# Performance work log

Hardware: AMD Instinct MI355X
Metric: run time of the kernel (lower is better)

The kernel has to match this reference:

```python
import jax, jax.numpy as jnp
import numpy as np

# LIF constants from the source module
ALPHA = float(np.exp(-0.001 / 0.005))  # synaptic decay
BETA = float(np.exp(-0.001 / 0.01))    # membrane decay
TH = 1.0
SCALE = 100.0

@jax.custom_vjp
def spike(x):
    return (x > 0).astype(x.dtype)

def _spike_fwd(x):
    return spike(x), x

def _spike_bwd(x, g):
    return (g / (1.0 + SCALE * jnp.abs(x)) ** 2,)

spike.defvjp(_spike_fwd, _spike_bwd)

T, NI, NH, NO = 1000, 700, 4096, 20

def setup_inputs() -> dict:
    key = jax.random.key(0)
    k1, k2, k3, k4 = jax.random.split(key, 4)
    input_spikes = (jax.random.uniform(k1, (T, NI)) < 0.1).astype(jnp.float32)
    # nn.Linear default init: U(-1/sqrt(fan_in), 1/sqrt(fan_in)), weight shape [out, in]
    s_in = 1.0 / np.sqrt(NI)
    s_fb = 1.0 / np.sqrt(NH)
    W_in = jax.random.uniform(k2, (NH, NI), minval=-s_in, maxval=s_in, dtype=jnp.float32)
    W_fb = jax.random.uniform(k3, (NH, NH), minval=-s_fb, maxval=s_fb, dtype=jnp.float32)
    W_ro = jax.random.uniform(k4, (NO, NH), minval=-s_fb, maxval=s_fb, dtype=jnp.float32)
    return {"input_spikes": input_spikes, "W_in": W_in, "W_fb": W_fb, "W_ro": W_ro}

def reference(input_spikes, W_in, W_fb, W_ro):
    nh = W_in.shape[0]
    no = W_ro.shape[0]

    def step(carry, inp):
        mem1, syn1, out1, mem2, syn2 = carry
        # input + feedback synaptic current (feedback uses previous step spikes)
        cur = W_in @ inp + W_fb @ out1
        # hidden LIF: reset where previous out spiked (detached), spike, decay
        rst = jax.lax.stop_gradient(out1)
        mem1 = mem1 * (1.0 - rst)
        out1_new = spike(mem1 - TH)
        mem1_new = mem1 * BETA + syn1
        syn1_new = syn1 * ALPHA + cur
        # readout LIF: no reset; recorded mem is pre-integration of current input
        ro_cur = W_ro @ out1_new
        mem2_new = mem2 * BETA + syn2
        syn2_new = syn2 * ALPHA + ro_cur
        return (mem1_new, syn1_new, out1_new, mem2_new, syn2_new), mem2_new

    carry0 = (jnp.zeros(nh, input_spikes.dtype), jnp.zeros(nh, input_spikes.dtype),
              jnp.zeros(nh, input_spikes.dtype), jnp.zeros(no, input_spikes.dtype),
              jnp.zeros(no, input_spikes.dtype))
    _, ro_mem_rec = jax.lax.scan(step, carry0, input_spikes)  # [T, num_output]
    return ro_mem_rec.T  # torch.stack(..., dim=1) -> [num_output, T]
```

## Files before the change

kernel.cpp:

```cpp
#include <hip/hip_runtime.h>

#define T_STEPS 1000
#define NI 700
#define NIQ 11
#define NH 4096
#define NO 20

#define ALPHA 0.8187307530779818f
#define BETA  0.9048374180359595f

#define NBH 64
#define BLOCK 1024
#define NWAVE 16
#define SPW 4
#define SLOTW 16
#define NCH 6
#define CAP (NCH * 8)
#define WLCAP 328
#define ZROW NI
#define NROWS (NI + 1 + NH)

typedef unsigned long long u64;
typedef unsigned int u32;
typedef int v4i __attribute__((ext_vector_type(4)));

__device__ __forceinline__ void pub16(u32* p, v4i v)
{
    asm volatile("global_store_dwordx4 %0, %1, off sc0 sc1"
                 :: "v"((u64)(uintptr_t)p), "v"(v) : "memory");
}
__device__ __forceinline__ v4i poll16(const u32* p)
{
    v4i r;
    asm volatile("global_load_dwordx4 %0, %1, off sc0 sc1\n\ts_waitcnt vmcnt(0)"
                 : "=v"(r) : "v"((u64)(uintptr_t)p) : "memory");
    return r;
}

__global__ void __launch_bounds__(256)
tpose_kernel(const float* __restrict__ in, float* __restrict__ out, int R, int C)
{
    __shared__ float tile[32][33];
    const int c  = blockIdx.x * 32 + threadIdx.x;
    const int r0 = blockIdx.y * 32;
    for (int dy = threadIdx.y; dy < 32; dy += 8) {
        const int r = r0 + dy;
        if (r < R && c < C) tile[dy][threadIdx.x] = in[(size_t)r * C + c];
    }
    __syncthreads();
    const int r2 = r0 + threadIdx.x;
    for (int dy = threadIdx.y; dy < 32; dy += 8) {
        const int c2 = blockIdx.x * 32 + dy;
        if (c2 < C && r2 < R) out[(size_t)c2 * R + r2] = tile[threadIdx.x][dy];
    }
}

__global__ void __launch_bounds__(256)
inpmask_kernel(const float* __restrict__ in, u64* __restrict__ msk)
{
    const int t    = blockIdx.x * 4 + (threadIdx.x >> 6);
    const int lane = threadIdx.x & 63;
    if (t >= T_STEPS) return;
    const float* __restrict__ row = in + (size_t)t * NI;
    for (int q = 0; q < NIQ; ++q) {
        const int j = q * 64 + lane;
        const u64 m = __ballot(j < NI && row[j] > 0.5f);
        if (lane == 0) msk[t * 16 + q] = m;
    }
}

__global__ void __launch_bounds__(BLOCK)
snn_kernel(const u64*  __restrict__ inpMask,
           const float* __restrict__ W_ro,
           const float* __restrict__ Wall,
           float* __restrict__ out,
           u32*   __restrict__ mb)
{
    const int tid  = threadIdx.x;
    const int lane = tid & 63;
    const int w    = tid >> 6;
    const int b    = blockIdx.x;

    if (b == NBH) {
        __shared__ int actR[NH];
        __shared__ int actRn;
        float mem2 = 0.f, syn2 = 0.f;

        for (int t = 0; t < T_STEPS; ++t) {
            if (w == 0) {
                const u32* tg = &mb[((size_t)t * NBH + lane) * SLOTW];
                v4i r;
                do { r = poll16(tg); } while ((u32)r.z != (u32)(t + 1));
                const u64 m = ((u64)(u32)r.y << 32) | (u32)r.x;
                const int cnt = __popcll(m);
                int v = cnt;
                #pragma unroll
                for (int d = 1; d < 64; d <<= 1) {
                    const int u = __shfl_up(v, d, 64);
                    if (lane >= d) v += u;
                }
                int o = v - cnt;
                if (lane == 63) actRn = v;
                u64 mm = m;
                const int base = lane * 64;
                while (mm) {
                    const int bit = __builtin_ctzll(mm);
                    mm &= mm - 1;
                    actR[o++] = base + bit;
                }
            }
            __syncthreads();

            const int nR = actRn;
            if (tid < NO * 32) {
                const int o = tid >> 5, k = tid & 31;
                const float* __restrict__ Wr = W_ro + o * NH;
                float r0 = 0.f, r1 = 0.f, r2 = 0.f, r3 = 0.f;
                int n = k;
                for (; n + 96 < nR; n += 128) {
                    r0 += Wr[actR[n]];      r1 += Wr[actR[n + 32]];
                    r2 += Wr[actR[n + 64]]; r3 += Wr[actR[n + 96]];
                }
                for (; n < nR; n += 32) r0 += Wr[actR[n]];
                float rc = (r0 + r1) + (r2 + r3);
                #pragma unroll
                for (int d = 16; d; d >>= 1) rc += __shfl_xor(rc, d, 32);
                if (k == 0) {
                    const float m2n = mem2 * BETA + syn2;
                    out[o * T_STEPS + t] = m2n;
                    syn2 = syn2 * ALPHA + rc;
                    mem2 = m2n;
                }
            }
            __syncthreads();
        }
        return;
    }

    __shared__ float pcur[2][BLOCK];
    __shared__ int   wl[2][NWAVE][WLCAP];

    const int i   = b * 64 + lane;
    const int bb0 = w * SPW;
    const int qw  = (w >= NWAVE - NIQ) ? (w - (NWAVE - NIQ)) : -1;
    const float* __restrict__ WallC = Wall + i;

    float M = 0.f, S = 0.f, o_prev = 0.f, o_cur = 0.f;
    float pf[CAP];
    int prevCnt = 0;

    if (w == 0 && lane == 0) {
        v4i pkt; pkt.x = 0; pkt.y = 0; pkt.z = 1; pkt.w = 0;
        pub16(&mb[(size_t)b * SLOTW], pkt);
    }

    for (int k = 0; k < T_STEPS; ++k) {
        const int pb = (k + 1) & 1;

        {
            float s0 = 0.f, s1 = 0.f, s2 = 0.f, s3 = 0.f;
            #pragma unroll
            for (int c = 0; c < NCH; ++c) {
                if (prevCnt > c * 8) {
                    s0 += pf[c*8+0]; s1 += pf[c*8+1];
                    s2 += pf[c*8+2]; s3 += pf[c*8+3];
                    s0 += pf[c*8+4]; s1 += pf[c*8+5];
                    s2 += pf[c*8+6]; s3 += pf[c*8+7];
                }
            }
            for (int n = CAP; n < prevCnt; ++n)
                s0 += WallC[(size_t)wl[pb & 1][w][n] * NH];
            pcur[pb][tid] = (s0 + s1) + (s2 + s3);
        }

        int cnt = 0;
        int* mylist = wl[k & 1][w];
        if (qw >= 0) {
            const u64 m = inpMask[(size_t)k * 16 + qw];
            if ((m >> lane) & 1)
                mylist[__popcll(m & (((u64)1 << lane) - 1))] = qw * 64 + lane;
            cnt = __popcll(m);
        }

        if (k > 0) {
            u64 mk = 0;
            if (lane < SPW) {
                const u32* tg = &mb[((size_t)(k - 1) * NBH + bb0 + lane) * SLOTW];
                v4i r;
                do { r = poll16(tg); } while ((u32)r.z != (u32)k);
                mk = ((u64)(u32)r.y << 32) | (u32)r.x;
            }
            #pragma unroll
            for (int s = 0; s < SPW; ++s) {
                const u64 m = __shfl(mk, s, 64);
                if ((m >> lane) & 1)
                    mylist[cnt + __popcll(m & (((u64)1 << lane) - 1))]
                        = NI + 1 + (bb0 + s) * 64 + lane;
                cnt += __popcll(m);
            }
        }
        const int padded = (cnt + 7) & ~7;
        if (lane < padded - cnt) mylist[cnt + lane] = ZROW;
        prevCnt = padded;

        #pragma unroll
        for (int c = 0; c < NCH; ++c) {
            if (padded > c * 8) {
                #pragma unroll
                for (int q = 0; q < 8; ++q)
                    pf[c*8+q] = WallC[(size_t)mylist[c*8+q] * NH];
            }
        }

        asm volatile("s_waitcnt lgkmcnt(0)\n\ts_barrier" ::: "memory");

        if (w == 0) {
            float cur = 0.f;
            #pragma unroll
            for (int ww = 0; ww < NWAVE; ++ww) cur += pcur[pb][lane + 64 * ww];
            S = S * ALPHA + cur;
            const float Mr = M * (1.f - o_prev);
            M = Mr * BETA + S;
            const float on = (M * (1.f - o_cur) > 1.f) ? 1.f : 0.f;
            o_prev = o_cur; o_cur = on;
            const u64 sm = __ballot(on > 0.f);
            if (lane == 0) {
                v4i pkt;
                pkt.x = (int)(u32)sm;
                pkt.y = (int)(u32)(sm >> 32);
                pkt.z = (int)(u32)(k + 2);
                pkt.w = 0;
                pub16(&mb[((size_t)(k + 1) * NBH + b) * SLOTW], pkt);
            }
        }
    }
}

extern "C" void kernel_launch(void* const* d_in, const int* in_sizes, int n_in,
                              void* d_out, int out_size, void* d_ws, size_t ws_size,
                              hipStream_t stream)
{
    const float* inp  = (const float*)d_in[0];
    const float* W_in = (const float*)d_in[1];
    const float* W_fb = (const float*)d_in[2];
    const float* W_ro = (const float*)d_in[3];
    float* out = (float*)d_out;

    char* ws = (char*)d_ws;
    size_t off = 0;
    auto alloc = [&](size_t bytes) -> void* {
        void* p = ws + off;
        off = (off + bytes + 255) & ~(size_t)255;
        return p;
    };
    float* Wall    = (float*)alloc(sizeof(float) * (size_t)NROWS * NH);
    u64*   inpMask = (u64*)alloc(sizeof(u64) * (size_t)T_STEPS * 16);
    u32*   mb      = (u32*)alloc(sizeof(u32) * (size_t)(T_STEPS + 1) * NBH * SLOTW);

    (void)hipMemsetAsync(mb, 0, sizeof(u32) * (size_t)(T_STEPS + 1) * NBH * SLOTW, stream);
    (void)hipMemsetAsync(Wall + (size_t)ZROW * NH, 0, sizeof(float) * NH, stream);

    dim3 tb(32, 8);
    tpose_kernel<<<dim3((NH + 31) / 32, (NH + 31) / 32), tb, 0, stream>>>(
        W_in, Wall, NH, NI);
    tpose_kernel<<<dim3((NH + 31) / 32, (NH + 31) / 32), tb, 0, stream>>>(
        W_fb, Wall + (size_t)(NI + 1) * NH, NH, NH);
    inpmask_kernel<<<(T_STEPS + 3) / 4, 256, 0, stream>>>(inp, inpMask);

    snn_kernel<<<NBH + 1, BLOCK, 0, stream>>>(inpMask, W_ro, Wall, out, mb);
}
```

Baseline: 3.708 ms.

## Dedicate wave 0 to LIF update and prefetch next-step mailbox polls

Wave 0 no longer gathers weight rows; it only reduces the partial currents and runs the LIF update. The 64 source blocks are redistributed over waves 1-15, four or five each. Each wave now issues the mailbox load for the next step before the barrier, so the spin-poll may already be satisfied when checked. Row indices are pre-shifted into element offsets and read as int4 from LDS, removing the per-gather multiply. This trades a little gather parallelism on wave 0 for a shorter critical path in the barrier-synchronised time loop.

```diff
diff --git a/kernel.cpp b/kernel.cpp
--- a/kernel.cpp
+++ b/kernel.cpp
@@ -12,12 +12,10 @@
 #define NBH 64
 #define BLOCK 1024
 #define NWAVE 16
-#define SPW 4
 #define SLOTW 16
 #define NCH 6
 #define CAP (NCH * 8)
 #define WLCAP 328
-#define ZROW NI
 #define NROWS (NI + 1 + NH)
 
 typedef unsigned long long u64;
@@ -140,14 +138,16 @@
     __shared__ float pcur[2][BLOCK];
     __shared__ int   wl[2][NWAVE][WLCAP];
 
-    const int i   = b * 64 + lane;
-    const int bb0 = w * SPW;
-    const int qw  = (w >= NWAVE - NIQ) ? (w - (NWAVE - NIQ)) : -1;
-    const float* __restrict__ WallC = Wall + i;
+    const int nsrc = (w == 0) ? 0 : (w <= 11 ? 4 : 5);
+    const int srcb = (w <= 11) ? (w - 1) * 4 : 44 + (w - 12) * 5;
+    const int qw   = (w >= 1 && w <= 11) ? (w - 1) : -1;
+    const int colv = b * 64 + lane;
+    const int ZOFF = NI << 12;
 
     float M = 0.f, S = 0.f, o_prev = 0.f, o_cur = 0.f;
     float pf[CAP];
     int prevCnt = 0;
+    v4i rpoll = {0, 0, 0, 0};
 
     if (w == 0 && lane == 0) {
         v4i pkt; pkt.x = 0; pkt.y = 0; pkt.z = 1; pkt.w = 0;
@@ -156,8 +156,18 @@
 
     for (int k = 0; k < T_STEPS; ++k) {
         const int pb = (k + 1) & 1;
-
-        {
+        int* mylist = wl[k & 1][w];
+        int cnt = 0;
+
+        if (qw >= 0) {
+            const u64 m = inpMask[(size_t)k * 16 + qw];
+            if ((m >> lane) & 1)
+                mylist[__popcll(m & (((u64)1 << lane) - 1))]
+                    = (qw * 64 + lane) << 12;
+            cnt = __popcll(m);
+        }
+
+        if (w) {
             float s0 = 0.f, s1 = 0.f, s2 = 0.f, s3 = 0.f;
             #pragma unroll
             for (int c = 0; c < NCH; ++c) {
@@ -168,48 +178,65 @@
                     s2 += pf[c*8+6]; s3 += pf[c*8+7];
                 }
             }
+            const int* wlPrev = wl[pb][w];
             for (int n = CAP; n < prevCnt; ++n)
-                s0 += WallC[(size_t)wl[pb & 1][w][n] * NH];
+                s0 += Wall[wlPrev[n] + colv];
             pcur[pb][tid] = (s0 + s1) + (s2 + s3);
         }
 
-        int cnt = 0;
-        int* mylist = wl[k & 1][w];
-        if (qw >= 0) {
-            const u64 m = inpMask[(size_t)k * 16 + qw];
-            if ((m >> lane) & 1)
-                mylist[__popcll(m & (((u64)1 << lane) - 1))] = qw * 64 + lane;
-            cnt = __popcll(m);
-        }
-
-        if (k > 0) {
+        if (w && k > 0) {
             u64 mk = 0;
-            if (lane < SPW) {
-                const u32* tg = &mb[((size_t)(k - 1) * NBH + bb0 + lane) * SLOTW];
-                v4i r;
-                do { r = poll16(tg); } while ((u32)r.z != (u32)k);
-                mk = ((u64)(u32)r.y << 32) | (u32)r.x;
-            }
-            #pragma unroll
-            for (int s = 0; s < SPW; ++s) {
-                const u64 m = __shfl(mk, s, 64);
-                if ((m >> lane) & 1)
-                    mylist[cnt + __popcll(m & (((u64)1 << lane) - 1))]
-                        = NI + 1 + (bb0 + s) * 64 + lane;
-                cnt += __popcll(m);
-            }
-        }
-        const int padded = (cnt + 7) & ~7;
-        if (lane < padded - cnt) mylist[cnt + lane] = ZROW;
-        prevCnt = padded;
-
-        #pragma unroll
-        for (int c = 0; c < NCH; ++c) {
-            if (padded > c * 8) {
-                #pragma unroll
-                for (int q = 0; q < 8; ++q)
-                    pf[c*8+q] = WallC[(size_t)mylist[c*8+q] * NH];
-            }
+            if (lane < nsrc) {
+                asm volatile("s_waitcnt vmcnt(0)" : "+v"(rpoll) :: "memory");
+                if ((u32)rpoll.z != (u32)k) {
+                    const u32* tg = &mb[((size_t)(k - 1) * NBH + srcb + lane) * SLOTW];
+                    v4i rr;
+                    do { rr = poll16(tg); } while ((u32)rr.z != (u32)k);
+                    rpoll = rr;
+                }
+                mk = ((u64)(u32)rpoll.y << 32) | (u32)rpoll.x;
+            }
+            #pragma unroll
+            for (int s = 0; s < 5; ++s) {
+                if (s < nsrc) {
+                    const u64 m = __shfl(mk, s, 64);
+                    if ((m >> lane) & 1)
+                        mylist[cnt + __popcll(m & (((u64)1 << lane) - 1))]
+                            = (NI + 1 + (srcb + s) * 64 + lane) << 12;
+                    cnt += __popcll(m);
+                }
+            }
+        }
+
+        int padded = 0;
+        if (w) {
+            padded = (cnt + 7) & ~7;
+            if (lane < padded - cnt) mylist[cnt + lane] = ZOFF;
+            prevCnt = padded;
+        }
+
+        if (w) {
+            #pragma unroll
+            for (int c = 0; c < NCH; ++c) {
+                if (padded > c * 8) {
+                    const int4 i0 = *(const int4*)&mylist[c*8];
+                    const int4 i1 = *(const int4*)&mylist[c*8+4];
+                    pf[c*8+0] = Wall[i0.x + colv];
+                    pf[c*8+1] = Wall[i0.y + colv];
+                    pf[c*8+2] = Wall[i0.z + colv];
+                    pf[c*8+3] = Wall[i0.w + colv];
+                    pf[c*8+4] = Wall[i1.x + colv];
+                    pf[c*8+5] = Wall[i1.y + colv];
+                    pf[c*8+6] = Wall[i1.z + colv];
+                    pf[c*8+7] = Wall[i1.w + colv];
+                }
+            }
+        }
+
+        if (w && lane < nsrc) {
+            const u64 pa = (u64)(uintptr_t)&mb[((size_t)k * NBH + srcb + lane) * SLOTW];
+            asm volatile("global_load_dwordx4 %0, %1, off sc0 sc1"
+                         : "=v"(rpoll) : "v"(pa) : "memory");
         }
 
         asm volatile("s_waitcnt lgkmcnt(0)\n\ts_barrier" ::: "memory");
@@ -217,7 +244,7 @@
         if (w == 0) {
             float cur = 0.f;
             #pragma unroll
-            for (int ww = 0; ww < NWAVE; ++ww) cur += pcur[pb][lane + 64 * ww];
+            for (int ww = 1; ww < NWAVE; ++ww) cur += pcur[pb][lane + 64 * ww];
             S = S * ALPHA + cur;
             const float Mr = M * (1.f - o_prev);
             M = Mr * BETA + S;
@@ -258,7 +285,7 @@
     u32*   mb      = (u32*)alloc(sizeof(u32) * (size_t)(T_STEPS + 1) * NBH * SLOTW);
 
     (void)hipMemsetAsync(mb, 0, sizeof(u32) * (size_t)(T_STEPS + 1) * NBH * SLOTW, stream);
-    (void)hipMemsetAsync(Wall + (size_t)ZROW * NH, 0, sizeof(float) * NH, stream);
+    (void)hipMemsetAsync(Wall + (size_t)NI * NH, 0, sizeof(float) * NH, stream);
 
     dim3 tb(32, 8);
     tpose_kernel<<<dim3((NH + 31) / 32, (NH + 31) / 32), tb, 0, stream>>>(
```

Measured after the change: 3.674 ms. No clear change (-0.9%).
